# Kernel optimization log

Hardware: AMD Instinct MI355X
Metric: run time of the kernel (lower is better)

Reference implementation:

```python
import jax, jax.numpy as jnp
import numpy as np

N = 4096
REG_STRENGTH = 1.0
BLOCK_EPS = 1e-6  # tolerance for detecting pooled-block boundaries in the backward


@jax.custom_vjp
def isotonic_l2(y):
    """argmin_{v_1 >= v_2 >= ... >= v_n} 0.5 * ||v - y||^2 (PAV solution).

    Computed via the exact minimax characterization, fully vectorized:
        v_i = min_{j <= i} max_{k >= i} mean(y[j..k])
    """
    return _iso_solution(y)


def _iso_solution(y):
    n = y.shape[0]
    cs = jnp.concatenate([jnp.zeros((1,), y.dtype), jnp.cumsum(y)])  # [n+1]
    idx = jnp.arange(n)
    j = idx[:, None]  # block start
    k = idx[None, :]  # block end
    length = (k - j + 1).astype(y.dtype)
    A = (cs[k + 1] - cs[j]) / length            # mean(y[j..k]) where k >= j
    A = jnp.where(k >= j, A, -jnp.inf)
    # M[j, i] = max_{k >= i} A[j, k]  (reverse cumulative max along k)
    M = jnp.flip(jax.lax.cummax(jnp.flip(A, axis=1), axis=1), axis=1)
    # v_i = min_{j <= i} M[j, i]  (cumulative min along j, take diagonal)
    v = jnp.diagonal(jax.lax.cummin(M, axis=0))
    return v


def _iso_fwd(y):
    v = _iso_solution(y)
    return v, v


def _iso_bwd(v, g):
    # Jacobian of PAV: within each pooled block, grad is the block mean of g.
    n = v.shape[0]
    drop = (v[:-1] - v[1:]) > BLOCK_EPS * jnp.maximum(jnp.abs(v[:-1]), 1.0)
    bid = jnp.concatenate([jnp.zeros((1,), jnp.int32),
                           jnp.cumsum(drop.astype(jnp.int32))])
    sums = jax.ops.segment_sum(g, bid, num_segments=n)
    cnts = jax.ops.segment_sum(jnp.ones_like(g), bid, num_segments=n)
    return ((sums / jnp.maximum(cnts, 1.0))[bid],)


isotonic_l2.defvjp(_iso_fwd, _iso_bwd)


def soft_rank(x, regularization_strength):
    """torchsort-style L2 soft rank: project x/eps onto permutahedron P([n..1])."""
    n = x.shape[0]
    theta = x / regularization_strength
    perm = jnp.argsort(-theta)          # descending sort permutation (constant wrt grad)
    s = theta[perm]
    w = jnp.arange(n, 0, -1, dtype=x.dtype)  # [n, n-1, ..., 1]
    sol = isotonic_l2(s - w)
    ranks_sorted = s - sol
    inv = jnp.argsort(perm)
    return ranks_sorted[inv]


def setup_inputs() -> dict:
    key = jax.random.key(0)
    kp, kt = jax.random.split(key)
    pred = jax.random.normal(kp, (N,), dtype=jnp.float32)
    target = jax.random.normal(kt, (N,), dtype=jnp.float32)
    return {"pred": pred, "target": target}


def reference(pred, target):
    p = soft_rank(pred, REG_STRENGTH)
    t = soft_rank(target, REG_STRENGTH)
    p = p - p.mean()
    p = p / jnp.linalg.norm(p)
    t = t - t.mean()
    t = t / jnp.linalg.norm(t)
    return 1.0 - jnp.sum(p * t)
```

## Files before the change

### kernel.cpp

```cpp
#include <hip/hip_runtime.h>
#include <math.h>

#define NEL   4096
#define NT    1024
#define HALF  512
#define EPT   8
#define CPT   4
#define JSEG  8
#define JLEN  (NEL / JSEG)
#define CB    256

#define WSYNC() asm volatile("s_waitcnt lgkmcnt(0)" ::: "memory")

__global__ __launch_bounds__(CB)
void count_kernel(const float* __restrict__ pred,
                  const float* __restrict__ target,
                  int* __restrict__ part) {
  __shared__ float jv[JLEN];
  const int arr = blockIdx.z;
  const float* __restrict__ x = arr ? target : pred;
  const int i     = blockIdx.x * CB + threadIdx.x;
  const int jbase = blockIdx.y * JLEN;

  for (int t = threadIdx.x; t < JLEN; t += CB) jv[t] = x[jbase + t];
  const float xi = x[i];
  __syncthreads();

  const float4* jv4 = (const float4*)jv;
  int c = 0;
#pragma unroll 4
  for (int t4 = 0; t4 < JLEN / 4; t4++) {
    const float4 v = jv4[t4];
    const int j = jbase + 4 * t4;
    c += (v.x > xi || (v.x == xi && j + 0 < i)) ? 1 : 0;
    c += (v.y > xi || (v.y == xi && j + 1 < i)) ? 1 : 0;
    c += (v.z > xi || (v.z == xi && j + 2 < i)) ? 1 : 0;
    c += (v.w > xi || (v.w == xi && j + 3 < i)) ? 1 : 0;
  }
  part[(arr * JSEG + blockIdx.y) * NEL + i] = c;
}

__device__ inline void pav_merge(double* P, int* C, const int lo, const int mid,
                                 const int hi) {
  const int llen = C[mid - 1];
  int cs = mid - llen;
  const int rlen = C[mid];
  int ce = mid + rlen - 1;
  const double mL = (P[mid] - P[cs]) / (double)llen;
  const double mR = (P[ce + 1] - P[mid]) / (double)rlen;
  if (mL <= mR) {
    double mu = (P[ce + 1] - P[cs]) / (double)(ce - cs + 1);
    bool changed = true;
    while (changed) {
      changed = false;
      while (cs > lo) {
        const int l2 = C[cs - 1];
        const double m2 = (P[cs] - P[cs - l2]) / (double)l2;
        if (m2 <= mu) {
          cs -= l2;
          mu = (P[ce + 1] - P[cs]) / (double)(ce - cs + 1);
          changed = true;
        } else break;
      }
      while (ce < hi - 1) {
        const int l2 = C[ce + 1];
        const double m2 = (P[ce + 1 + l2] - P[ce + 1]) / (double)l2;
        if (m2 >= mu) {
          ce += l2;
          mu = (P[ce + 1] - P[cs]) / (double)(ce - cs + 1);
          changed = true;
        } else break;
      }
    }
    const int len = ce - cs + 1;
    C[cs] = len;
    C[ce] = len;
  }
}

__global__ __launch_bounds__(NT)
void pav_loss_kernel(const float* __restrict__ pred,
                     const float* __restrict__ target,
                     const int* __restrict__ part,
                     float* __restrict__ loss_out) {
  __shared__ float  s_val[2][NEL];
  __shared__ double s_P[2][NEL + 1];
  __shared__ int    s_cnt[2][NEL];
  __shared__ double s_wsum[2][HALF / 64];
  __shared__ int    s_nb[2];
  __shared__ double s_red[NT / 64][5];

  const int tid  = threadIdx.x;
  const int lane = tid & 63;
  const int wid  = tid >> 6;

  int rp[CPT], rt[CPT];
  {
    const int4* p4 = (const int4*)part;
    int4 a = make_int4(0, 0, 0, 0), b = make_int4(0, 0, 0, 0);
#pragma unroll
    for (int s = 0; s < JSEG; s++) {
      const int4 u = p4[s * (NEL / 4) + tid];
      a.x += u.x; a.y += u.y; a.z += u.z; a.w += u.w;
      const int4 v = p4[(JSEG + s) * (NEL / 4) + tid];
      b.x += v.x; b.y += v.y; b.z += v.z; b.w += v.w;
    }
    rp[0] = a.x; rp[1] = a.y; rp[2] = a.z; rp[3] = a.w;
    rt[0] = b.x; rt[1] = b.y; rt[2] = b.z; rt[3] = b.w;
    const float4 xp = ((const float4*)pred)[tid];
    const float4 xt = ((const float4*)target)[tid];
    s_val[0][rp[0]] = xp.x; s_val[0][rp[1]] = xp.y;
    s_val[0][rp[2]] = xp.z; s_val[0][rp[3]] = xp.w;
    s_val[1][rt[0]] = xt.x; s_val[1][rt[1]] = xt.y;
    s_val[1][rt[2]] = xt.z; s_val[1][rt[3]] = xt.w;
  }
  __syncthreads();

  const int arr = tid >> 9;
  const int tA  = tid & (HALF - 1);
  const int wA  = tA >> 6;
  const int b0  = tA * EPT;
  double* P = s_P[arr];
  int*    C = s_cnt[arr];

  double c[EPT];
  {
    double acc = 0.0;
#pragma unroll
    for (int e = 0; e < EPT; e++) {
      const int p = b0 + e;
      acc += (double)s_val[arr][p] - (double)(NEL - p);
      c[e] = acc;
    }
  }
  const double tot = c[EPT - 1];
  double sc = tot;
#pragma unroll
  for (int d = 1; d < 64; d <<= 1) {
    const double o = __shfl_up(sc, d, 64);
    if (lane >= d) sc += o;
  }
  if (lane == 63) s_wsum[arr][wA] = sc;
  __syncthreads();
  double wexcl = 0.0;
#pragma unroll
  for (int w = 0; w < HALF / 64; w++)
    wexcl += (w < wA) ? s_wsum[arr][w] : 0.0;
  const double excl = wexcl + (sc - tot);
#pragma unroll
  for (int e = 0; e < EPT; e++) P[b0 + 1 + e] = excl + c[e];
  if (lane == 0) P[b0] = excl;

  C[b0] = 1;
  for (int p = b0 + 1; p < b0 + EPT; p++) {
    int cs = p;
    const double Pe = P[p + 1];
    while (cs > b0) {
      const int l2 = C[cs - 1];
      const int lb = cs - l2;
      const double Pcs = P[cs];
      const double Plb = (lb == b0) ? excl : P[lb];
      const double mPrev = (Pcs - Plb) / (double)l2;
      const double mCur  = (Pe - Pcs) / (double)(p - cs + 1);
      if (mPrev <= mCur) cs = lb; else break;
    }
    C[cs] = p - cs + 1;
    C[p]  = p - cs + 1;
  }
  WSYNC();

  const int wbase = wA * 512;
#pragma unroll
  for (int m = EPT; m <= 256; m <<= 1) {
    const int nm = 512 / (2 * m);
    if (lane < nm) {
      const int lo = wbase + lane * 2 * m;
      pav_merge(P, C, lo, lo + m, lo + 2 * m);
    }
    WSYNC();
  }
  __syncthreads();

  if (wA == 0) {
#pragma unroll
    for (int m = 512; m <= 2048; m <<= 1) {
      const int nm = NEL / (2 * m);
      if (lane < nm) {
        const int lo = lane * 2 * m;
        pav_merge(P, C, lo, lo + m, lo + 2 * m);
      }
      WSYNC();
    }
    if (lane == 0) {
      int s = 0, b = 0;
      while (s < NEL) {
        const int cc = C[s];
        C[b] = s;
        b++;
        s += cc;
      }
      s_nb[arr] = b;
    }
  }
  __syncthreads();

  const int nb = s_nb[arr];
#pragma unroll
  for (int e = 0; e < EPT; e++) {
    const int p = b0 + e;
    int lo = 0, hi = nb - 1;
    while (lo < hi) {
      const int md = (lo + hi + 1) >> 1;
      if (C[md] <= p) lo = md; else hi = md - 1;
    }
    const int st = C[lo];
    const int en = (lo + 1 < nb) ? C[lo + 1] : NEL;
    const double v = (P[en] - P[st]) / (double)(en - st);
    s_val[arr][p] = (float)((double)s_val[arr][p] - v);
  }
  __syncthreads();

  double Sp = 0.0, Sq = 0.0, Spp = 0.0, Sqq = 0.0, Spq = 0.0;
#pragma unroll
  for (int e = 0; e < CPT; e++) {
    const double p = (double)s_val[0][rp[e]];
    const double q = (double)s_val[1][rt[e]];
    Sp += p; Sq += q; Spp += p * p; Sqq += q * q; Spq += p * q;
  }
#pragma unroll
  for (int d = 32; d > 0; d >>= 1) {
    Sp  += __shfl_down(Sp,  d, 64);
    Sq  += __shfl_down(Sq,  d, 64);
    Spp += __shfl_down(Spp, d, 64);
    Sqq += __shfl_down(Sqq, d, 64);
    Spq += __shfl_down(Spq, d, 64);
  }
  if (lane == 0) {
    s_red[wid][0] = Sp;  s_red[wid][1] = Sq;  s_red[wid][2] = Spp;
    s_red[wid][3] = Sqq; s_red[wid][4] = Spq;
  }
  __syncthreads();
  if (tid == 0) {
    double a0 = 0, a1 = 0, a2 = 0, a3 = 0, a4 = 0;
    for (int w = 0; w < NT / 64; w++) {
      a0 += s_red[w][0]; a1 += s_red[w][1]; a2 += s_red[w][2];
      a3 += s_red[w][3]; a4 += s_red[w][4];
    }
    const double n  = (double)NEL;
    const double mp = a0 / n, mq = a1 / n;
    const double cov = a4 - n * mp * mq;
    const double vp  = a2 - n * mp * mp;
    const double vq  = a3 - n * mq * mq;
    loss_out[0] = (float)(1.0 - cov / sqrt(vp * vq));
  }
}

extern "C" void kernel_launch(void* const* d_in, const int* in_sizes, int n_in,
                              void* d_out, int out_size, void* d_ws, size_t ws_size,
                              hipStream_t stream) {
  const float* pred   = (const float*)d_in[0];
  const float* target = (const float*)d_in[1];
  int*   part = (int*)d_ws;
  float* out  = (float*)d_out;

  hipLaunchKernelGGL(count_kernel, dim3(NEL / CB, JSEG, 2), dim3(CB), 0,
                     stream, pred, target, part);
  hipLaunchKernelGGL(pav_loss_kernel, dim3(1), dim3(NT), 0, stream,
                     pred, target, part, out);
}
```

Baseline: 92.45 us.

## Use atomic rank counts, padded LDS indexing, division-free PAV merges, minimax leaf blocks

The rank-count kernel now splits the j dimension into 16 segments of 256 elements and accumulates counts with atomicAdd into a zeroed buffer (an added memset). This removes the 8-way partial-sum buffer and the reduction loop in the main kernel. LDS arrays for values and prefix sums are padded (p + p/8) to cut bank conflicts. PAV merge comparisons are cross-multiplied to avoid double divisions. The sequential per-thread leaf PAV is replaced by a fully unrolled register-only minimax computation. Costs are an extra memset launch, many more small blocks with atomics, and heavier unrolled register code.

```diff
diff --git a/kernel.cpp b/kernel.cpp
--- a/kernel.cpp
+++ b/kernel.cpp
@@ -6,38 +6,38 @@
 #define HALF  512
 #define EPT   8
 #define CPT   4
-#define JSEG  8
-#define JLEN  (NEL / JSEG)
 #define CB    256
+
+#define IX(p) ((p) + ((p) >> 3))
 
 #define WSYNC() asm volatile("s_waitcnt lgkmcnt(0)" ::: "memory")
 
 __global__ __launch_bounds__(CB)
 void count_kernel(const float* __restrict__ pred,
                   const float* __restrict__ target,
-                  int* __restrict__ part) {
-  __shared__ float jv[JLEN];
+                  unsigned int* __restrict__ counts) {
+  __shared__ float jv[CB];
   const int arr = blockIdx.z;
   const float* __restrict__ x = arr ? target : pred;
   const int i     = blockIdx.x * CB + threadIdx.x;
-  const int jbase = blockIdx.y * JLEN;
-
-  for (int t = threadIdx.x; t < JLEN; t += CB) jv[t] = x[jbase + t];
+  const int jbase = blockIdx.y * CB;
+
+  jv[threadIdx.x] = x[jbase + threadIdx.x];
   const float xi = x[i];
   __syncthreads();
 
   const float4* jv4 = (const float4*)jv;
-  int c = 0;
+  unsigned int c = 0;
 #pragma unroll 4
-  for (int t4 = 0; t4 < JLEN / 4; t4++) {
+  for (int t4 = 0; t4 < CB / 4; t4++) {
     const float4 v = jv4[t4];
     const int j = jbase + 4 * t4;
-    c += (v.x > xi || (v.x == xi && j + 0 < i)) ? 1 : 0;
-    c += (v.y > xi || (v.y == xi && j + 1 < i)) ? 1 : 0;
-    c += (v.z > xi || (v.z == xi && j + 2 < i)) ? 1 : 0;
-    c += (v.w > xi || (v.w == xi && j + 3 < i)) ? 1 : 0;
-  }
-  part[(arr * JSEG + blockIdx.y) * NEL + i] = c;
+    c += (v.x > xi || (v.x == xi && j + 0 < i)) ? 1u : 0u;
+    c += (v.y > xi || (v.y == xi && j + 1 < i)) ? 1u : 0u;
+    c += (v.z > xi || (v.z == xi && j + 2 < i)) ? 1u : 0u;
+    c += (v.w > xi || (v.w == xi && j + 3 < i)) ? 1u : 0u;
+  }
+  atomicAdd(&counts[arr * NEL + i], c);
 }
 
 __device__ inline void pav_merge(double* P, int* C, const int lo, const int mid,
@@ -46,29 +46,24 @@
   int cs = mid - llen;
   const int rlen = C[mid];
   int ce = mid + rlen - 1;
-  const double mL = (P[mid] - P[cs]) / (double)llen;
-  const double mR = (P[ce + 1] - P[mid]) / (double)rlen;
-  if (mL <= mR) {
-    double mu = (P[ce + 1] - P[cs]) / (double)(ce - cs + 1);
+  const double Pmid = P[IX(mid)];
+  double Pcs = P[IX(cs)], Pce1 = P[IX(ce + 1)];
+  if ((Pmid - Pcs) * (double)rlen <= (Pce1 - Pmid) * (double)llen) {
     bool changed = true;
     while (changed) {
       changed = false;
       while (cs > lo) {
         const int l2 = C[cs - 1];
-        const double m2 = (P[cs] - P[cs - l2]) / (double)l2;
-        if (m2 <= mu) {
-          cs -= l2;
-          mu = (P[ce + 1] - P[cs]) / (double)(ce - cs + 1);
-          changed = true;
+        const double Pl = P[IX(cs - l2)];
+        if ((Pcs - Pl) * (double)(ce - cs + 1) <= (Pce1 - Pcs) * (double)l2) {
+          cs -= l2; Pcs = Pl; changed = true;
         } else break;
       }
       while (ce < hi - 1) {
         const int l2 = C[ce + 1];
-        const double m2 = (P[ce + 1 + l2] - P[ce + 1]) / (double)l2;
-        if (m2 >= mu) {
-          ce += l2;
-          mu = (P[ce + 1] - P[cs]) / (double)(ce - cs + 1);
-          changed = true;
+        const double Pr = P[IX(ce + 1 + l2)];
+        if ((Pr - Pce1) * (double)(ce - cs + 1) >= (Pce1 - Pcs) * (double)l2) {
+          ce += l2; Pce1 = Pr; changed = true;
         } else break;
       }
     }
@@ -81,10 +76,10 @@
 __global__ __launch_bounds__(NT)
 void pav_loss_kernel(const float* __restrict__ pred,
                      const float* __restrict__ target,
-                     const int* __restrict__ part,
+                     const unsigned int* __restrict__ counts,
                      float* __restrict__ loss_out) {
-  __shared__ float  s_val[2][NEL];
-  __shared__ double s_P[2][NEL + 1];
+  __shared__ float  s_val[2][IX(NEL - 1) + 2];
+  __shared__ double s_P[2][IX(NEL) + 1];
   __shared__ int    s_cnt[2][NEL];
   __shared__ double s_wsum[2][HALF / 64];
   __shared__ int    s_nb[2];
@@ -96,23 +91,16 @@
 
   int rp[CPT], rt[CPT];
   {
-    const int4* p4 = (const int4*)part;
-    int4 a = make_int4(0, 0, 0, 0), b = make_int4(0, 0, 0, 0);
-#pragma unroll
-    for (int s = 0; s < JSEG; s++) {
-      const int4 u = p4[s * (NEL / 4) + tid];
-      a.x += u.x; a.y += u.y; a.z += u.z; a.w += u.w;
-      const int4 v = p4[(JSEG + s) * (NEL / 4) + tid];
-      b.x += v.x; b.y += v.y; b.z += v.z; b.w += v.w;
-    }
-    rp[0] = a.x; rp[1] = a.y; rp[2] = a.z; rp[3] = a.w;
-    rt[0] = b.x; rt[1] = b.y; rt[2] = b.z; rt[3] = b.w;
+    const uint4 a = ((const uint4*)counts)[tid];
+    const uint4 b = ((const uint4*)counts)[NEL / 4 + tid];
+    rp[0] = (int)a.x; rp[1] = (int)a.y; rp[2] = (int)a.z; rp[3] = (int)a.w;
+    rt[0] = (int)b.x; rt[1] = (int)b.y; rt[2] = (int)b.z; rt[3] = (int)b.w;
     const float4 xp = ((const float4*)pred)[tid];
     const float4 xt = ((const float4*)target)[tid];
-    s_val[0][rp[0]] = xp.x; s_val[0][rp[1]] = xp.y;
-    s_val[0][rp[2]] = xp.z; s_val[0][rp[3]] = xp.w;
-    s_val[1][rt[0]] = xt.x; s_val[1][rt[1]] = xt.y;
-    s_val[1][rt[2]] = xt.z; s_val[1][rt[3]] = xt.w;
+    s_val[0][IX(rp[0])] = xp.x; s_val[0][IX(rp[1])] = xp.y;
+    s_val[0][IX(rp[2])] = xp.z; s_val[0][IX(rp[3])] = xp.w;
+    s_val[1][IX(rt[0])] = xt.x; s_val[1][IX(rt[1])] = xt.y;
+    s_val[1][IX(rt[2])] = xt.z; s_val[1][IX(rt[3])] = xt.w;
   }
   __syncthreads();
 
@@ -129,7 +117,7 @@
 #pragma unroll
     for (int e = 0; e < EPT; e++) {
       const int p = b0 + e;
-      acc += (double)s_val[arr][p] - (double)(NEL - p);
+      acc += (double)s_val[arr][IX(p)] - (double)(NEL - p);
       c[e] = acc;
     }
   }
@@ -148,24 +136,63 @@
     wexcl += (w < wA) ? s_wsum[arr][w] : 0.0;
   const double excl = wexcl + (sc - tot);
 #pragma unroll
-  for (int e = 0; e < EPT; e++) P[b0 + 1 + e] = excl + c[e];
-  if (lane == 0) P[b0] = excl;
-
-  C[b0] = 1;
-  for (int p = b0 + 1; p < b0 + EPT; p++) {
-    int cs = p;
-    const double Pe = P[p + 1];
-    while (cs > b0) {
-      const int l2 = C[cs - 1];
-      const int lb = cs - l2;
-      const double Pcs = P[cs];
-      const double Plb = (lb == b0) ? excl : P[lb];
-      const double mPrev = (Pcs - Plb) / (double)l2;
-      const double mCur  = (Pe - Pcs) / (double)(p - cs + 1);
-      if (mPrev <= mCur) cs = lb; else break;
-    }
-    C[cs] = p - cs + 1;
-    C[p]  = p - cs + 1;
+  for (int e = 0; e < EPT; e++) P[IX(b0 + 1 + e)] = excl + c[e];
+  if (lane == 0) P[IX(b0)] = excl;
+
+  double nmx[EPT]; int dmx[EPT];
+  double vn[EPT];  int vd[EPT];
+  {
+#pragma unroll
+    for (int j = 0; j < EPT; j++) {
+      nmx[j] = c[7] - (j ? c[j - 1] : 0.0);
+      dmx[j] = EPT - j;
+    }
+    double mn = nmx[0]; int md = dmx[0];
+#pragma unroll
+    for (int j = 1; j < EPT; j++)
+      if (nmx[j] * (double)md < mn * (double)dmx[j]) { mn = nmx[j]; md = dmx[j]; }
+    vn[7] = mn; vd[7] = md;
+#pragma unroll
+    for (int p = EPT - 2; p >= 0; p--) {
+#pragma unroll
+      for (int j = 0; j < EPT - 1; j++) {
+        if (j <= p) {
+          const double cnum = c[p] - (j ? c[j - 1] : 0.0);
+          const int cden = p - j + 1;
+          if (cnum * (double)dmx[j] > nmx[j] * (double)cden) {
+            nmx[j] = cnum; dmx[j] = cden;
+          }
+        }
+      }
+      double mn2 = nmx[0]; int md2 = dmx[0];
+#pragma unroll
+      for (int j = 1; j < EPT - 1; j++) {
+        if (j <= p) {
+          if (nmx[j] * (double)md2 < mn2 * (double)dmx[j]) {
+            mn2 = nmx[j]; md2 = dmx[j];
+          }
+        }
+      }
+      vn[p] = mn2; vd[p] = md2;
+    }
+  }
+  {
+    int runstart = b0;
+#pragma unroll
+    for (int e = 1; e < EPT; e++) {
+      const bool neq = (vd[e] != vd[e - 1]) ||
+                       (__double_as_longlong(vn[e]) !=
+                        __double_as_longlong(vn[e - 1]));
+      if (neq) {
+        const int len = b0 + e - runstart;
+        C[runstart] = len;
+        C[b0 + e - 1] = len;
+        runstart = b0 + e;
+      }
+    }
+    const int len = b0 + EPT - runstart;
+    C[runstart] = len;
+    C[b0 + EPT - 1] = len;
   }
   WSYNC();
 
@@ -215,16 +242,16 @@
     }
     const int st = C[lo];
     const int en = (lo + 1 < nb) ? C[lo + 1] : NEL;
-    const double v = (P[en] - P[st]) / (double)(en - st);
-    s_val[arr][p] = (float)((double)s_val[arr][p] - v);
+    const double v = (P[IX(en)] - P[IX(st)]) / (double)(en - st);
+    s_val[arr][IX(p)] = (float)((double)s_val[arr][IX(p)] - v);
   }
   __syncthreads();
 
   double Sp = 0.0, Sq = 0.0, Spp = 0.0, Sqq = 0.0, Spq = 0.0;
 #pragma unroll
   for (int e = 0; e < CPT; e++) {
-    const double p = (double)s_val[0][rp[e]];
-    const double q = (double)s_val[1][rt[e]];
+    const double p = (double)s_val[0][IX(rp[e])];
+    const double q = (double)s_val[1][IX(rt[e])];
     Sp += p; Sq += q; Spp += p * p; Sqq += q * q; Spq += p * q;
   }
 #pragma unroll
@@ -260,11 +287,12 @@
                               hipStream_t stream) {
   const float* pred   = (const float*)d_in[0];
   const float* target = (const float*)d_in[1];
-  int*   part = (int*)d_ws;
-  float* out  = (float*)d_out;
-
-  hipLaunchKernelGGL(count_kernel, dim3(NEL / CB, JSEG, 2), dim3(CB), 0,
-                     stream, pred, target, part);
+  unsigned int* counts = (unsigned int*)d_ws;
+  float* out = (float*)d_out;
+
+  hipMemsetAsync(counts, 0, 2 * NEL * sizeof(unsigned int), stream);
+  hipLaunchKernelGGL(count_kernel, dim3(NEL / CB, NEL / CB, 2), dim3(CB), 0,
+                     stream, pred, target, counts);
   hipLaunchKernelGGL(pav_loss_kernel, dim3(1), dim3(NT), 0, stream,
-                     pred, target, part, out);
-}
+                     pred, target, counts, out);
+}
```

Measured after the change: 80.52 us. 12.9% less time.
